# Kernel optimization log

Hardware: AMD Instinct MI355X
Metric: run time of the kernel (lower is better)

## Reference

```python
import jax, jax.numpy as jnp
import numpy as np

N = 50000   # total nodes
E = 600000  # total edges
F = 128     # in_features == hidden_features
H = 128
L = 4       # layers_count
B = 256     # number of graphs in batch
M = 200     # molecule_features
OUT = 12    # out_features
MH = H // 4 # molecular head width


def setup_inputs() -> dict:
    key = jax.random.key(0)
    ks = jax.random.split(key, 16)
    x = jax.random.normal(ks[0], (N, F), dtype=jnp.float32)
    edge_index = jax.random.randint(ks[1], (2, E), 0, N, dtype=jnp.int64)
    # sorted segment ids; guarantee every graph has >=1 node
    batch = jnp.sort(jnp.concatenate([
        jnp.arange(B, dtype=jnp.int64),
        jax.random.randint(ks[2], (N - B,), 0, B, dtype=jnp.int64)]))
    molecule_features = jax.random.normal(ks[3], (B, M), dtype=jnp.float32)
    s = 0.05
    Ws = jax.random.normal(ks[4], (L, H, H), dtype=jnp.float32) * s
    bs = jnp.zeros((L, H), dtype=jnp.float32)
    Wm = jax.random.normal(ks[5], (M, MH), dtype=jnp.float32) * s
    bm = jnp.zeros((MH,), dtype=jnp.float32)
    gamma = jnp.ones((MH,), dtype=jnp.float32)   # BatchNorm1d affine (eval mode, running stats 0/1)
    beta = jnp.zeros((MH,), dtype=jnp.float32)
    W1 = jax.random.normal(ks[6], (2 * H + MH, H), dtype=jnp.float32) * s  # mlp in = 288
    b1 = jnp.zeros((H,), dtype=jnp.float32)
    W2 = jax.random.normal(ks[7], (H, OUT), dtype=jnp.float32) * s
    b2 = jnp.zeros((OUT,), dtype=jnp.float32)
    return dict(x=x, edge_index=edge_index, batch=batch,
                molecule_features=molecule_features, Ws=Ws, bs=bs,
                Wm=Wm, bm=bm, gamma=gamma, beta=beta,
                W1=W1, b1=b1, W2=W2, b2=b2)


def gcn_conv(x, src, dst, W, b):
    # GCNConv: D^{-1/2} (A + I) D^{-1/2} X W + b, degrees include self loops
    ones = jnp.ones((E,), dtype=x.dtype)
    deg = jax.ops.segment_sum(ones, dst, num_segments=N) + 1.0  # self loop
    dis = jax.lax.rsqrt(deg)
    norm = dis[src] * dis[dst]                      # [E]
    xw = x @ W                                      # [N,H]
    msg = xw[src] * norm[:, None]                   # gather + scale
    agg = jax.ops.segment_sum(msg, dst, num_segments=N)
    agg = agg + xw * (dis * dis)[:, None]           # self-loop term
    return agg + b


def reference(x, edge_index, batch, molecule_features, Ws, bs, Wm, bm,
              gamma, beta, W1, b1, W2, b2):
    src, dst = edge_index[0], edge_index[1]
    h = x
    for l in range(L):
        y = jax.nn.relu(gcn_conv(h, src, dst, Ws[l], bs[l]))
        h = y + h  # residual (in == hidden); dropout is identity in eval
    max_pool = jax.ops.segment_max(h, batch, num_segments=B)
    add_pool = jax.ops.segment_sum(h, batch, num_segments=B)
    # molecular head: Linear -> Dropout(eval=identity) -> BatchNorm1d(eval) -> ReLU
    mol = molecule_features @ Wm + bm
    mol = jax.nn.relu(mol * gamma + beta)  # running_mean=0, running_var=1
    z = jnp.concatenate((max_pool, add_pool, mol), axis=1)  # [B, 288]
    z = jax.nn.relu(z @ W1 + b1)
    return z @ W2 + b2  # [B, OUT]
```

## Files before the change

kernel.cpp:

```cpp
#include <hip/hip_runtime.h>
#include <hip/hip_fp16.h>
#include <math.h>

static constexpr int NN  = 50000;
static constexpr int NE  = 600000;
static constexpr int HD  = 128;
static constexpr int NL  = 4;
static constexpr int NB  = 256;
static constexpr int NM  = 200;
static constexpr int NO  = 12;
static constexpr int NMH = 32;

#define MAX4(ac, b) { (ac).x = fmaxf((ac).x,(b).x); (ac).y = fmaxf((ac).y,(b).y); (ac).z = fmaxf((ac).z,(b).z); (ac).w = fmaxf((ac).w,(b).w); }
#define ADD4(ac, b) { (ac).x += (b).x; (ac).y += (b).y; (ac).z += (b).z; (ac).w += (b).w; }

typedef short bfx8 __attribute__((ext_vector_type(8)));
typedef float f32x4 __attribute__((ext_vector_type(4)));

__device__ __forceinline__ unsigned short f2bf(float f) {
  unsigned int u = __float_as_uint(f);
  unsigned int r = (u + 0x7fffu + ((u >> 16) & 1u)) >> 16;
  return (unsigned short)r;
}
__device__ __forceinline__ float bflo(unsigned int p) { return __uint_as_float(p << 16); }
__device__ __forceinline__ float bfhi(unsigned int p) { return __uint_as_float(p & 0xffff0000u); }
__device__ __forceinline__ float h2f_hi(unsigned e) {
  return __half2float(__ushort_as_half((unsigned short)(e >> 16)));
}

__global__ void k_hist(const int* __restrict__ dst, int* __restrict__ counts) {
  int e = blockIdx.x * blockDim.x + threadIdx.x;
  if (e < NE) atomicAdd(&counts[dst[e]], 1);
}

__global__ void k_scan1(const int* __restrict__ counts, int* __restrict__ incl,
                        int* __restrict__ bsum, float* __restrict__ dis) {
  __shared__ int s[256];
  int i = blockIdx.x * 256 + threadIdx.x;
  int v = (i < NN) ? counts[i] : 0;
  if (i < NN) dis[i] = rsqrtf((float)(v + 1));
  s[threadIdx.x] = v;
  __syncthreads();
  for (int off = 1; off < 256; off <<= 1) {
    int t = (threadIdx.x >= off) ? s[threadIdx.x - off] : 0;
    __syncthreads();
    s[threadIdx.x] += t;
    __syncthreads();
  }
  if (i < NN) incl[i] = s[threadIdx.x];
  if (threadIdx.x == 255) bsum[blockIdx.x] = s[255];
}

__global__ void k_scan2(const int* __restrict__ bsum, int* __restrict__ boff, int nblocks) {
  __shared__ int s[256];
  int v = (threadIdx.x < nblocks) ? bsum[threadIdx.x] : 0;
  s[threadIdx.x] = v;
  __syncthreads();
  for (int off = 1; off < 256; off <<= 1) {
    int t = (threadIdx.x >= off) ? s[threadIdx.x - off] : 0;
    __syncthreads();
    s[threadIdx.x] += t;
    __syncthreads();
  }
  boff[threadIdx.x] = s[threadIdx.x] - v;
}

__global__ void k_scan3(const int* __restrict__ counts, int* __restrict__ rowst, const int* __restrict__ boff) {
  int i = blockIdx.x * 256 + threadIdx.x;
  if (i < NN) {
    rowst[i] = rowst[i] - counts[i] + boff[blockIdx.x];
    if (i == NN - 1) rowst[NN] = NE;
  }
}

__global__ void k_fill(const int* __restrict__ src, const int* __restrict__ dst,
                       const int* __restrict__ rowst, const float* __restrict__ dis,
                       int* __restrict__ cur, unsigned* __restrict__ csr) {
  int e = blockIdx.x * blockDim.x + threadIdx.x;
  if (e < NE) {
    int d = dst[e];
    int s = src[e];
    int p = atomicAdd(&cur[d], 1);
    unsigned hb = (unsigned)__half_as_ushort(__float2half(dis[s]));
    csr[rowst[d] + p] = (hb << 16) | (unsigned)s;
  }
}

__global__ void k_goffs(const int* __restrict__ batch, int* __restrict__ goffs) {
  int i = blockIdx.x * blockDim.x + threadIdx.x;
  if (i >= NN) return;
  int b = batch[i];
  if (i == 0) {
    for (int g = 0; g <= b; ++g) goffs[g] = 0;
  } else {
    int pb = batch[i - 1];
    for (int g = pb + 1; g <= b; ++g) goffs[g] = i;
  }
  if (i == NN - 1) goffs[NB] = NN;
}

__global__ void k_tobf(const float4* __restrict__ in, ushort4* __restrict__ outb, int n4) {
  int i = blockIdx.x * blockDim.x + threadIdx.x;
  if (i < n4) {
    float4 v = in[i];
    outb[i] = make_ushort4(f2bf(v.x), f2bf(v.y), f2bf(v.z), f2bf(v.w));
  }
}

__global__ void k_wT(const float* __restrict__ Ws, unsigned short* __restrict__ wT) {
  int i = blockIdx.x * blockDim.x + threadIdx.x;
  if (i < NL * HD * HD) {
    int l = i >> 14, rem = i & 16383, n = rem >> 7, k = rem & 127;
    wT[i] = f2bf(Ws[l * 16384 + k * 128 + n]);
  }
}

__launch_bounds__(256)
__global__ void k_gemm_mfma(const unsigned short* __restrict__ A,
                            const unsigned short* __restrict__ WT,
                            unsigned short* __restrict__ C) {
  const int wave = threadIdx.x >> 6;
  const int lane = threadIdx.x & 63;
  const int m_base = blockIdx.x * 128 + wave * 32;
  const int lr = lane & 15;
  const int kg = lane >> 4;

  f32x4 acc[2][8];
#pragma unroll
  for (int mi = 0; mi < 2; ++mi)
#pragma unroll
    for (int nj = 0; nj < 8; ++nj) acc[mi][nj] = (f32x4){0.f, 0.f, 0.f, 0.f};

  int ra0 = m_base + lr;       if (ra0 > NN - 1) ra0 = NN - 1;
  int ra1 = m_base + 16 + lr;  if (ra1 > NN - 1) ra1 = NN - 1;

#pragma unroll
  for (int kb = 0; kb < 4; ++kb) {
    const int k0 = kb * 32 + kg * 8;
    bfx8 a0 = *(const bfx8*)&A[(size_t)ra0 * HD + k0];
    bfx8 a1 = *(const bfx8*)&A[(size_t)ra1 * HD + k0];
#pragma unroll
    for (int nj = 0; nj < 8; ++nj) {
      bfx8 b = *(const bfx8*)&WT[(nj * 16 + lr) * HD + k0];
      acc[0][nj] = __builtin_amdgcn_mfma_f32_16x16x32_bf16(a0, b, acc[0][nj], 0, 0, 0);
      acc[1][nj] = __builtin_amdgcn_mfma_f32_16x16x32_bf16(a1, b, acc[1][nj], 0, 0, 0);
    }
  }

  const int col = lane & 15;
  const int rbase = (lane >> 4) * 4;
#pragma unroll
  for (int mi = 0; mi < 2; ++mi) {
#pragma unroll
    for (int r = 0; r < 4; ++r) {
      int row = m_base + mi * 16 + rbase + r;
      if (row < NN) {
#pragma unroll
        for (int nj = 0; nj < 8; ++nj) {
          C[(size_t)row * HD + nj * 16 + col] = f2bf(acc[mi][nj][r]);
        }
      }
    }
  }
}

#define AGG_EDGE(e, p) { float nm = h2f_hi(e) * dn; \
    acc.x += nm * bflo((p).x); acc.y += nm * bfhi((p).x); \
    acc.z += nm * bflo((p).y); acc.w += nm * bfhi((p).y); }

__global__ void k_agg(const unsigned short* __restrict__ xw, const float* __restrict__ dis,
                      const int* __restrict__ rowst, const unsigned* __restrict__ csr,
                      const float* __restrict__ bias, const unsigned short* __restrict__ hinb,
                      unsigned short* __restrict__ houtb) {
  int g = threadIdx.x >> 5;
  int lane = threadIdx.x & 31;
  int n = blockIdx.x * 8 + g;
  if (n >= NN) return;

  const uint2* xwb = (const uint2*)xw;

  float dn = dis[n];
  float4 acc;
  {
    uint2 p = xwb[(size_t)n * 32 + lane];
    float sl = dn * dn;
    acc.x = bflo(p.x) * sl; acc.y = bfhi(p.x) * sl;
    acc.z = bflo(p.y) * sl; acc.w = bfhi(p.y) * sl;
  }

  int s0 = rowst[n], s1 = rowst[n + 1];
  int idx = s0;
  for (; idx + 8 <= s1; idx += 8) {
    unsigned e0 = csr[idx],     e1 = csr[idx + 1], e2 = csr[idx + 2], e3 = csr[idx + 3];
    unsigned e4 = csr[idx + 4], e5 = csr[idx + 5], e6 = csr[idx + 6], e7 = csr[idx + 7];
    uint2 p0 = xwb[(size_t)(e0 & 0xffffu) * 32 + lane];
    uint2 p1 = xwb[(size_t)(e1 & 0xffffu) * 32 + lane];
    uint2 p2 = xwb[(size_t)(e2 & 0xffffu) * 32 + lane];
    uint2 p3 = xwb[(size_t)(e3 & 0xffffu) * 32 + lane];
    uint2 p4 = xwb[(size_t)(e4 & 0xffffu) * 32 + lane];
    uint2 p5 = xwb[(size_t)(e5 & 0xffffu) * 32 + lane];
    uint2 p6 = xwb[(size_t)(e6 & 0xffffu) * 32 + lane];
    uint2 p7 = xwb[(size_t)(e7 & 0xffffu) * 32 + lane];
    AGG_EDGE(e0, p0); AGG_EDGE(e1, p1); AGG_EDGE(e2, p2); AGG_EDGE(e3, p3);
    AGG_EDGE(e4, p4); AGG_EDGE(e5, p5); AGG_EDGE(e6, p6); AGG_EDGE(e7, p7);
  }
  for (; idx + 4 <= s1; idx += 4) {
    unsigned e0 = csr[idx], e1 = csr[idx + 1], e2 = csr[idx + 2], e3 = csr[idx + 3];
    uint2 p0 = xwb[(size_t)(e0 & 0xffffu) * 32 + lane];
    uint2 p1 = xwb[(size_t)(e1 & 0xffffu) * 32 + lane];
    uint2 p2 = xwb[(size_t)(e2 & 0xffffu) * 32 + lane];
    uint2 p3 = xwb[(size_t)(e3 & 0xffffu) * 32 + lane];
    AGG_EDGE(e0, p0); AGG_EDGE(e1, p1); AGG_EDGE(e2, p2); AGG_EDGE(e3, p3);
  }
  for (; idx < s1; ++idx) {
    unsigned e0 = csr[idx];
    uint2 p0 = xwb[(size_t)(e0 & 0xffffu) * 32 + lane];
    AGG_EDGE(e0, p0);
  }

  float4 b4 = *(const float4*)&bias[lane * 4];
  uint2 hp = ((const uint2*)hinb)[(size_t)n * 32 + lane];
  float4 outv;
  outv.x = fmaxf(acc.x + b4.x, 0.f) + bflo(hp.x);
  outv.y = fmaxf(acc.y + b4.y, 0.f) + bfhi(hp.x);
  outv.z = fmaxf(acc.z + b4.z, 0.f) + bflo(hp.y);
  outv.w = fmaxf(acc.w + b4.w, 0.f) + bfhi(hp.y);
  *(ushort4*)&houtb[(size_t)n * HD + lane * 4] =
      make_ushort4(f2bf(outv.x), f2bf(outv.y), f2bf(outv.z), f2bf(outv.w));
}

__launch_bounds__(1024)
__global__ void k_pool(const unsigned short* __restrict__ hb, const int* __restrict__ goffs,
                       float* __restrict__ pooled) {
  __shared__ float4 smax[32][32];
  __shared__ float4 ssum[32][32];
  int g = blockIdx.x;
  int slot = threadIdx.x >> 5;
  int lane = threadIdx.x & 31;
  int a = goffs[g], bnd = goffs[g + 1];
  const uint2* hb2 = (const uint2*)hb;

  float4 mx = make_float4(-INFINITY, -INFINITY, -INFINITY, -INFINITY);
  float4 sm = make_float4(0.f, 0.f, 0.f, 0.f);
  for (int i = a + slot; i < bnd; i += 32) {
    uint2 p = hb2[(size_t)i * 32 + lane];
    float4 v = make_float4(bflo(p.x), bfhi(p.x), bflo(p.y), bfhi(p.y));
    MAX4(mx, v);
    ADD4(sm, v);
  }
  smax[slot][lane] = mx;
  ssum[slot][lane] = sm;
  __syncthreads();
#pragma unroll
  for (int off = 16; off >= 1; off >>= 1) {
    if (slot < off) {
      float4 m2 = smax[slot + off][lane];
      float4 s2 = ssum[slot + off][lane];
      float4 m1 = smax[slot][lane];
      float4 s1 = ssum[slot][lane];
      MAX4(m1, m2);
      ADD4(s1, s2);
      smax[slot][lane] = m1;
      ssum[slot][lane] = s1;
    }
    __syncthreads();
  }
  if (slot == 0) {
    *(float4*)&pooled[g * 256 + lane * 4]       = smax[0][lane];
    *(float4*)&pooled[g * 256 + 128 + lane * 4] = ssum[0][lane];
  }
}

__global__ void k_head(const float* __restrict__ pooled, const float* __restrict__ mf,
                       const float* __restrict__ Wm, const float* __restrict__ bm,
                       const float* __restrict__ gamma, const float* __restrict__ beta,
                       const float* __restrict__ W1, const float* __restrict__ b1,
                       const float* __restrict__ W2, const float* __restrict__ b2,
                       float* __restrict__ out) {
  __shared__ float z[288];
  __shared__ float z1[128];
  int g = blockIdx.x, t = threadIdx.x;
  z[t] = pooled[g * 256 + t];
  z[128 + t] = pooled[g * 256 + 128 + t];
  if (t < NMH) {
    float acc = bm[t];
    for (int k = 0; k < NM; ++k) acc += mf[g * NM + k] * Wm[k * NMH + t];
    acc = acc * gamma[t] + beta[t];
    z[256 + t] = fmaxf(acc, 0.f);
  }
  __syncthreads();
  float acc = b1[t];
  for (int k = 0; k < 288; ++k) acc += z[k] * W1[k * HD + t];
  z1[t] = fmaxf(acc, 0.f);
  __syncthreads();
  if (t < NO) {
    float a2 = b2[t];
    for (int k = 0; k < HD; ++k) a2 += z1[k] * W2[k * NO + t];
    out[g * NO + t] = a2;
  }
}

extern "C" void kernel_launch(void* const* d_in, const int* in_sizes, int n_in,
                              void* d_out, int out_size, void* d_ws, size_t ws_size,
                              hipStream_t stream) {
  const float* x     = (const float*)d_in[0];
  const int*   eidx  = (const int*)d_in[1];
  const int*   batch = (const int*)d_in[2];
  const float* mf    = (const float*)d_in[3];
  const float* Ws    = (const float*)d_in[4];
  const float* bs    = (const float*)d_in[5];
  const float* Wm    = (const float*)d_in[6];
  const float* bm    = (const float*)d_in[7];
  const float* gamma = (const float*)d_in[8];
  const float* beta  = (const float*)d_in[9];
  const float* W1    = (const float*)d_in[10];
  const float* b1    = (const float*)d_in[11];
  const float* W2    = (const float*)d_in[12];
  const float* b2    = (const float*)d_in[13];
  float* out = (float*)d_out;

  const int* src = eidx;
  const int* dst = eidx + NE;

  char* w = (char*)d_ws;
  size_t off = 0;
  auto alloc = [&](size_t bytes) -> void* {
    void* p = w + off;
    off += (bytes + 255) & ~(size_t)255;
    return p;
  };
  float* dis    = (float*)alloc((size_t)NN * 4);
  unsigned short* xw  = (unsigned short*)alloc((size_t)NN * HD * 2);
  unsigned short* xbf = (unsigned short*)alloc((size_t)NN * HD * 2);
  unsigned short* hbf = (unsigned short*)alloc((size_t)NN * HD * 2);
  unsigned short* wT  = (unsigned short*)alloc((size_t)NL * HD * HD * 2);
  int* counts   = (int*)alloc((size_t)NN * 4);
  int* cur      = (int*)alloc((size_t)NN * 4);
  int* rowst    = (int*)alloc((size_t)(NN + 1) * 4);
  unsigned* csr = (unsigned*)alloc((size_t)NE * 4);
  int* bsum     = (int*)alloc(256 * 4);
  int* boff     = (int*)alloc(256 * 4);
  int* goffs    = (int*)alloc((size_t)(NB + 1) * 4);
  float* pooled = (float*)alloc((size_t)NB * 256 * 4);
  (void)ws_size;

  const int SB = (NN + 255) / 256;

  hipMemsetAsync(counts, 0, (size_t)NN * 4, stream);
  hipMemsetAsync(cur, 0, (size_t)NN * 4, stream);

  k_hist<<<(NE + 255) / 256, 256, 0, stream>>>(dst, counts);
  k_scan1<<<SB, 256, 0, stream>>>(counts, rowst, bsum, dis);
  k_scan2<<<1, 256, 0, stream>>>(bsum, boff, SB);
  k_scan3<<<SB, 256, 0, stream>>>(counts, rowst, boff);
  k_fill<<<(NE + 255) / 256, 256, 0, stream>>>(src, dst, rowst, dis, cur, csr);

  k_goffs<<<SB, 256, 0, stream>>>(batch, goffs);
  k_tobf<<<((NN * HD / 4) + 255) / 256, 256, 0, stream>>>((const float4*)x, (ushort4*)xbf, NN * HD / 4);
  k_wT<<<(NL * HD * HD + 255) / 256, 256, 0, stream>>>(Ws, wT);

  for (int l = 0; l < NL; ++l) {
    const unsigned short* gin_bf = (l == 0) ? xbf : hbf;
    k_gemm_mfma<<<(NN + 127) / 128, 256, 0, stream>>>(gin_bf, wT + (size_t)l * HD * HD, xw);
    k_agg<<<(NN + 7) / 8, 256, 0, stream>>>(xw, dis, rowst, csr, bs + (size_t)l * HD, gin_bf, hbf);
  }

  k_pool<<<NB, 1024, 0, stream>>>(hbf, goffs, pooled);
  k_head<<<NB, 128, 0, stream>>>(pooled, mf, Wm, bm, gamma, beta, W1, b1, W2, b2, out);
}
```

Measured before the change: 283.0 us.

## Split GCN aggregation into two feature-half passes to shrink gather working set

The neighbour aggregation kernel now handles one 64-feature half of each node per launch, using 16 lanes per node and 16 nodes per block. It is launched twice per layer, once per half. Each pass gathers from a half-width slice of xw, so the randomly accessed working set shrinks and should sit better in the L2 and last-level caches. In exchange, the CSR index and degree reads are done twice, there is an extra launch per layer, and each gather touches only 128 bytes per row.

```diff
diff --git a/kernel.cpp b/kernel.cpp
--- a/kernel.cpp
+++ b/kernel.cpp
@@ -168,21 +168,23 @@
     acc.x += nm * bflo((p).x); acc.y += nm * bfhi((p).x); \
     acc.z += nm * bflo((p).y); acc.w += nm * bfhi((p).y); }
 
-__global__ void k_agg(const unsigned short* __restrict__ xw, const float* __restrict__ dis,
-                      const int* __restrict__ rowst, const unsigned* __restrict__ csr,
-                      const float* __restrict__ bias, const unsigned short* __restrict__ hinb,
-                      unsigned short* __restrict__ houtb) {
-  int g = threadIdx.x >> 5;
-  int lane = threadIdx.x & 31;
-  int n = blockIdx.x * 8 + g;
+__launch_bounds__(256)
+__global__ void k_agg_h(const unsigned short* __restrict__ xw, const float* __restrict__ dis,
+                        const int* __restrict__ rowst, const unsigned* __restrict__ csr,
+                        const float* __restrict__ bias, const unsigned short* __restrict__ hinb,
+                        unsigned short* __restrict__ houtb, int fh) {
+  int slot = threadIdx.x >> 4;
+  int lane = threadIdx.x & 15;
+  int n = blockIdx.x * 16 + slot;
   if (n >= NN) return;
 
   const uint2* xwb = (const uint2*)xw;
+  const int fo = fh * 16 + lane;
 
   float dn = dis[n];
   float4 acc;
   {
-    uint2 p = xwb[(size_t)n * 32 + lane];
+    uint2 p = xwb[(size_t)n * 32 + fo];
     float sl = dn * dn;
     acc.x = bflo(p.x) * sl; acc.y = bfhi(p.x) * sl;
     acc.z = bflo(p.y) * sl; acc.w = bfhi(p.y) * sl;
@@ -193,39 +195,39 @@
   for (; idx + 8 <= s1; idx += 8) {
     unsigned e0 = csr[idx],     e1 = csr[idx + 1], e2 = csr[idx + 2], e3 = csr[idx + 3];
     unsigned e4 = csr[idx + 4], e5 = csr[idx + 5], e6 = csr[idx + 6], e7 = csr[idx + 7];
-    uint2 p0 = xwb[(size_t)(e0 & 0xffffu) * 32 + lane];
-    uint2 p1 = xwb[(size_t)(e1 & 0xffffu) * 32 + lane];
-    uint2 p2 = xwb[(size_t)(e2 & 0xffffu) * 32 + lane];
-    uint2 p3 = xwb[(size_t)(e3 & 0xffffu) * 32 + lane];
-    uint2 p4 = xwb[(size_t)(e4 & 0xffffu) * 32 + lane];
-    uint2 p5 = xwb[(size_t)(e5 & 0xffffu) * 32 + lane];
-    uint2 p6 = xwb[(size_t)(e6 & 0xffffu) * 32 + lane];
-    uint2 p7 = xwb[(size_t)(e7 & 0xffffu) * 32 + lane];
+    uint2 p0 = xwb[(size_t)(e0 & 0xffffu) * 32 + fo];
+    uint2 p1 = xwb[(size_t)(e1 & 0xffffu) * 32 + fo];
+    uint2 p2 = xwb[(size_t)(e2 & 0xffffu) * 32 + fo];
+    uint2 p3 = xwb[(size_t)(e3 & 0xffffu) * 32 + fo];
+    uint2 p4 = xwb[(size_t)(e4 & 0xffffu) * 32 + fo];
+    uint2 p5 = xwb[(size_t)(e5 & 0xffffu) * 32 + fo];
+    uint2 p6 = xwb[(size_t)(e6 & 0xffffu) * 32 + fo];
+    uint2 p7 = xwb[(size_t)(e7 & 0xffffu) * 32 + fo];
     AGG_EDGE(e0, p0); AGG_EDGE(e1, p1); AGG_EDGE(e2, p2); AGG_EDGE(e3, p3);
     AGG_EDGE(e4, p4); AGG_EDGE(e5, p5); AGG_EDGE(e6, p6); AGG_EDGE(e7, p7);
   }
   for (; idx + 4 <= s1; idx += 4) {
     unsigned e0 = csr[idx], e1 = csr[idx + 1], e2 = csr[idx + 2], e3 = csr[idx + 3];
-    uint2 p0 = xwb[(size_t)(e0 & 0xffffu) * 32 + lane];
-    uint2 p1 = xwb[(size_t)(e1 & 0xffffu) * 32 + lane];
-    uint2 p2 = xwb[(size_t)(e2 & 0xffffu) * 32 + lane];
-    uint2 p3 = xwb[(size_t)(e3 & 0xffffu) * 32 + lane];
+    uint2 p0 = xwb[(size_t)(e0 & 0xffffu) * 32 + fo];
+    uint2 p1 = xwb[(size_t)(e1 & 0xffffu) * 32 + fo];
+    uint2 p2 = xwb[(size_t)(e2 & 0xffffu) * 32 + fo];
+    uint2 p3 = xwb[(size_t)(e3 & 0xffffu) * 32 + fo];
     AGG_EDGE(e0, p0); AGG_EDGE(e1, p1); AGG_EDGE(e2, p2); AGG_EDGE(e3, p3);
   }
   for (; idx < s1; ++idx) {
     unsigned e0 = csr[idx];
-    uint2 p0 = xwb[(size_t)(e0 & 0xffffu) * 32 + lane];
+    uint2 p0 = xwb[(size_t)(e0 & 0xffffu) * 32 + fo];
     AGG_EDGE(e0, p0);
   }
 
-  float4 b4 = *(const float4*)&bias[lane * 4];
-  uint2 hp = ((const uint2*)hinb)[(size_t)n * 32 + lane];
+  float4 b4 = *(const float4*)&bias[fh * 64 + lane * 4];
+  uint2 hp = ((const uint2*)hinb)[(size_t)n * 32 + fo];
   float4 outv;
   outv.x = fmaxf(acc.x + b4.x, 0.f) + bflo(hp.x);
   outv.y = fmaxf(acc.y + b4.y, 0.f) + bfhi(hp.x);
   outv.z = fmaxf(acc.z + b4.z, 0.f) + bflo(hp.y);
   outv.w = fmaxf(acc.w + b4.w, 0.f) + bfhi(hp.y);
-  *(ushort4*)&houtb[(size_t)n * HD + lane * 4] =
+  ((ushort4*)houtb)[(size_t)n * 32 + fo] =
       make_ushort4(f2bf(outv.x), f2bf(outv.y), f2bf(outv.z), f2bf(outv.w));
 }
 
@@ -359,10 +361,12 @@
   k_tobf<<<((NN * HD / 4) + 255) / 256, 256, 0, stream>>>((const float4*)x, (ushort4*)xbf, NN * HD / 4);
   k_wT<<<(NL * HD * HD + 255) / 256, 256, 0, stream>>>(Ws, wT);
 
+  const int AB = (NN + 15) / 16;
   for (int l = 0; l < NL; ++l) {
     const unsigned short* gin_bf = (l == 0) ? xbf : hbf;
     k_gemm_mfma<<<(NN + 127) / 128, 256, 0, stream>>>(gin_bf, wT + (size_t)l * HD * HD, xw);
-    k_agg<<<(NN + 7) / 8, 256, 0, stream>>>(xw, dis, rowst, csr, bs + (size_t)l * HD, gin_bf, hbf);
+    k_agg_h<<<AB, 256, 0, stream>>>(xw, dis, rowst, csr, bs + (size_t)l * HD, gin_bf, hbf, 0);
+    k_agg_h<<<AB, 256, 0, stream>>>(xw, dis, rowst, csr, bs + (size_t)l * HD, gin_bf, hbf, 1);
   }
 
   k_pool<<<NB, 1024, 0, stream>>>(hbf, goffs, pooled);
```

After: 302.7 us. 1.07x slower.
